# Kernel tuning notes

Hardware: AMD Instinct MI355X
Metric: run time of the kernel (lower is better)

Reference implementation:

```python
import jax, jax.numpy as jnp
import numpy as np

N_NODES = 50000
N_EDGES = 800000
NODE_DIM = 128
EDGE_DIM = 64
HIDDEN = 256


def setup_inputs() -> dict:
    key = jax.random.key(0)
    ks = jax.random.split(key, 12)
    glorot = lambda k, fi, fo: jax.random.normal(k, (fi, fo), jnp.float32) * (2.0 / (fi + fo)) ** 0.5
    return {
        "node_features": jax.random.normal(ks[0], (N_NODES, NODE_DIM), jnp.float32),
        "edge_features": jax.random.normal(ks[1], (N_EDGES, EDGE_DIM), jnp.float32),
        "src": jax.random.randint(ks[2], (N_EDGES,), 0, N_NODES),
        "dst": jax.random.randint(ks[3], (N_EDGES,), 0, N_NODES),
        # edge_update MLP: (2*node_dim + edge_dim) -> hidden -> edge_dim
        "We1": glorot(ks[4], 2 * NODE_DIM + EDGE_DIM, HIDDEN),
        "be1": jnp.zeros((HIDDEN,), jnp.float32),
        "We2": glorot(ks[5], HIDDEN, EDGE_DIM),
        "be2": jnp.zeros((EDGE_DIM,), jnp.float32),
        # node_update MLP: (node_dim + edge_dim) -> hidden -> node_dim
        "Wn1": glorot(ks[6], NODE_DIM + EDGE_DIM, HIDDEN),
        "bn1": jnp.zeros((HIDDEN,), jnp.float32),
        "Wn2": glorot(ks[7], HIDDEN, NODE_DIM),
        "bn2": jnp.zeros((NODE_DIM,), jnp.float32),
    }


def reference(node_features, edge_features, src, dst, We1, be1, We2, be2, Wn1, bn1, Wn2, bn2):
    # message: per-edge MLP on [src_h, e, dst_h]
    concat = jnp.concatenate(
        [node_features[src], edge_features, node_features[dst]], axis=1
    )  # [E, 2*node_dim + edge_dim]
    e_upd = jax.nn.relu(concat @ We1 + be1) @ We2 + be2  # [E, edge_dim]

    # reduce: sum incoming messages per destination node
    e_sum = jax.ops.segment_sum(e_upd, dst, num_segments=node_features.shape[0])  # [N, edge_dim]
    node_in = jnp.concatenate([node_features, e_sum], axis=1)  # [N, node_dim + edge_dim]
    h_new = jax.nn.relu(node_in @ Wn1 + bn1) @ Wn2 + bn2  # [N, node_dim]

    # DGL only applies reduce_func to nodes with at least one incoming edge
    deg = jax.ops.segment_sum(jnp.ones_like(dst, jnp.float32), dst, num_segments=node_features.shape[0])
    h_out = jnp.where(deg[:, None] > 0, h_new, node_features)

    # original module never writes e_updated back: returned edge features are the inputs
    return h_out, edge_features
```

## Files before the change

### kernel.cpp

```cpp
#include <hip/hip_runtime.h>

#define N_NODES 50000
#define N_EDGES 800000
#define NODE_DIM 128
#define EDGE_DIM 64
#define HIDDEN 256
#define K_N 192

typedef __attribute__((ext_vector_type(8))) short bf16x8;
typedef __attribute__((ext_vector_type(4))) float f32x4;
typedef __attribute__((ext_vector_type(16))) float f32x16;
typedef unsigned short u16;
typedef unsigned int u32;

#define MFMA16 __builtin_amdgcn_mfma_f32_16x16x32_bf16
#define MFMA32 __builtin_amdgcn_mfma_f32_32x32x16_bf16

__device__ inline u16 f2bf(float f) {
  u32 u = __builtin_bit_cast(u32, f);
  u += 0x7fffu + ((u >> 16) & 1u);
  return (u16)(u >> 16);
}
__device__ inline float bf2f(u16 u) {
  u32 x = ((u32)u) << 16;
  return __builtin_bit_cast(float, x);
}
__device__ inline u32 cvt_pk(float a, float b) {
  u32 r;
  asm("v_cvt_pk_bf16_f32 %0, %1, %2" : "=v"(r) : "v"(a), "v"(b));
  return r;
}
__device__ inline void st_bf4(u16* p, float4 v) {
  ushort4 r;
  r.x = f2bf(v.x); r.y = f2bf(v.y); r.z = f2bf(v.z); r.w = f2bf(v.w);
  *reinterpret_cast<ushort4*>(p) = r;
}

__global__ void prep_weights(const float* __restrict__ We1, const float* __restrict__ We2,
                             const float* __restrict__ Wn1, const float* __restrict__ Wn2,
                             const float* __restrict__ be2, const int* __restrict__ dst,
                             u16* __restrict__ w1st, u16* __restrict__ w1dt,
                             u16* __restrict__ w1ef, u16* __restrict__ w2y,
                             u16* __restrict__ wn1t, u16* __restrict__ wn2t,
                             float* __restrict__ b2p, int* __restrict__ hist) {
  const int stride = gridDim.x * blockDim.x;
  const int tid = blockIdx.x * blockDim.x + threadIdx.x;
  for (int i = tid; i < HIDDEN * NODE_DIM; i += stride) {
    int h = i >> 7, k = i & 127;
    w1st[i] = f2bf(We1[k * HIDDEN + h]);
    w1dt[i] = f2bf(We1[(192 + k) * HIDDEN + h]);
  }
  for (int i = tid; i < 8 * 4 * 64 * 8; i += stride) {
    int jj = i & 7;
    int l = (i >> 3) & 63;
    int kb = (i >> 9) & 3;
    int ht = i >> 11;
    int h = ht * 32 + (l & 31);
    int kloc = kb * 16 + (l >> 5) * 8 + jj;
    w1ef[i] = f2bf(We1[(128 + kloc) * HIDDEN + h]);
  }
  for (int i = tid; i < EDGE_DIM * HIDDEN; i += stride) {
    int jj = i & 7;
    int l = (i >> 3) & 63;
    int t2 = (i >> 9) & 1;
    int kb2 = i >> 10;
    int out = t2 * 32 + (l & 31);
    int hi = l >> 5;
    int k = kb2 * 16 + (jj & 3) + 8 * (jj >> 2) + 4 * hi;
    w2y[i] = f2bf(We2[k * EDGE_DIM + out]);
  }
  for (int i = tid; i < HIDDEN * K_N; i += stride) {
    int n = i / K_N, k = i % K_N;
    wn1t[i] = f2bf(Wn1[k * HIDDEN + n]);
  }
  for (int i = tid; i < NODE_DIM * HIDDEN; i += stride) {
    int n = i / HIDDEN, k = i % HIDDEN;
    wn2t[i] = f2bf(Wn2[k * NODE_DIM + n]);
  }
  for (int i = tid; i < EDGE_DIM; i += stride) {
    int t2 = i >> 5, hi = (i >> 4) & 1, r = i & 15;
    b2p[i] = be2[t2 * 32 + (r & 3) + 8 * (r >> 2) + 4 * hi];
  }
  for (int i = tid; i < N_EDGES; i += stride)
    atomicAdd(&hist[dst[i]], 1);
}

#define NB_P 782
#define SA_P 136
#define SH   264

__global__ __launch_bounds__(256) void pgemm_kernel(
    const float* __restrict__ nf, const u16* __restrict__ w1st,
    const u16* __restrict__ w1dt, const float* __restrict__ be1,
    u16* __restrict__ P_src, u16* __restrict__ P_dst)
{
  __shared__ u16 A[64 * SA_P];
  __shared__ u16 H[64 * SH];
  const int tid = threadIdx.x;
  const int n0 = blockIdx.x * 64;
  const float4* nf4 = reinterpret_cast<const float4*>(nf);

  #pragma unroll
  for (int p = 0; p < 8; ++p) {
    int i = p * 256 + tid;
    int row = i >> 5, c4 = i & 31;
    int rg = min(n0 + row, N_NODES - 1);
    float4 v = nf4[(size_t)rg * 32 + c4];
    st_bf4(&A[row * SA_P + c4 * 4], v);
  }
  __syncthreads();

  const int wave = tid >> 6, lane = tid & 63;
  const int lr = lane & 15;
  const int lk = (lane >> 4) * 8;

  for (int table = 0; table < 2; ++table) {
    const u16* w = table ? w1dt : w1st;
    u16* P = table ? P_dst : P_src;

    f32x4 acc[4][4] = {};
    #pragma unroll
    for (int kb = 0; kb < 4; ++kb) {
      const int ko = kb * 32 + lk;
      bf16x8 a[4], bb[4];
      #pragma unroll
      for (int mt = 0; mt < 4; ++mt)
        a[mt] = *reinterpret_cast<const bf16x8*>(&A[(mt * 16 + lr) * SA_P + ko]);
      #pragma unroll
      for (int nt = 0; nt < 4; ++nt)
        bb[nt] = *reinterpret_cast<const bf16x8*>(&w[(size_t)(wave * 64 + nt * 16 + lr) * 128 + ko]);
      #pragma unroll
      for (int mt = 0; mt < 4; ++mt)
        #pragma unroll
        for (int nt = 0; nt < 4; ++nt)
          acc[mt][nt] = MFMA16(a[mt], bb[nt], acc[mt][nt], 0, 0, 0);
    }
    __syncthreads();

    #pragma unroll
    for (int mt = 0; mt < 4; ++mt)
      #pragma unroll
      for (int nt = 0; nt < 4; ++nt) {
        int col = wave * 64 + nt * 16 + lr;
        float bias = table ? 0.f : be1[col];
        #pragma unroll
        for (int j = 0; j < 4; ++j) {
          int row = mt * 16 + (lane >> 4) * 4 + j;
          H[row * SH + col] = f2bf(acc[mt][nt][j] + bias);
        }
      }
    __syncthreads();

    #pragma unroll
    for (int p = 0; p < 16; ++p) {
      int u = p * 256 + tid;
      int row = u >> 6, cg = u & 63;
      int hi = cg >> 5, ht = (cg >> 2) & 7, q = cg & 3;
      int hbase = ht * 32 + 8 * q + 4 * hi;
      int n = n0 + row;
      if (n < N_NODES) {
        ushort4 v = *reinterpret_cast<const ushort4*>(&H[row * SH + hbase]);
        *reinterpret_cast<ushort4*>(&P[(size_t)n * 256 + cg * 4]) = v;
      }
    }
  }
}

#define NB_SCAN 196

__global__ void scanA_kernel(const int* __restrict__ hist, int* __restrict__ eid) {
  __shared__ int red[256];
  int gid = blockIdx.x * 256 + threadIdx.x;
  int v = (gid < N_NODES) ? hist[gid] : 0;
  red[threadIdx.x] = v;
  __syncthreads();
  for (int d = 128; d > 0; d >>= 1) {
    if (threadIdx.x < d) red[threadIdx.x] += red[threadIdx.x + d];
    __syncthreads();
  }
  if (threadIdx.x == 0) eid[blockIdx.x] = red[0];
}

__global__ void scanB_kernel(int* __restrict__ eid, int* __restrict__ off) {
  __shared__ int ssum[256];
  int tid = threadIdx.x;
  int v = (tid < NB_SCAN) ? eid[tid] : 0;
  ssum[tid] = v;
  __syncthreads();
  for (int d = 1; d < 256; d <<= 1) {
    int t = (tid >= d) ? ssum[tid - d] : 0;
    __syncthreads();
    ssum[tid] += t;
    __syncthreads();
  }
  if (tid < NB_SCAN) eid[256 + tid] = ssum[tid] - v;
  if (tid == 255) off[N_NODES] = ssum[255];
}

__global__ void scanC_kernel(const int* __restrict__ hist, const int* __restrict__ eid,
                             int* __restrict__ off, int* __restrict__ cursor,
                             float* __restrict__ e_sum) {
  __shared__ int ssum[256];
  int tid = threadIdx.x;
  int gid = blockIdx.x * 256 + tid;
  int base = eid[256 + blockIdx.x];
  int v = (gid < N_NODES) ? hist[gid] : 0;
  ssum[tid] = v;
  __syncthreads();
  for (int d = 1; d < 256; d <<= 1) {
    int t = (tid >= d) ? ssum[tid - d] : 0;
    __syncthreads();
    ssum[tid] += t;
    __syncthreads();
  }
  if (gid < N_NODES) {
    int o = base + ssum[tid] - v;
    off[gid] = o;
    cursor[gid] = o;
    float4 z = {0.f, 0.f, 0.f, 0.f};
    float4* ez = reinterpret_cast<float4*>(e_sum + (size_t)gid * 64);
    #pragma unroll
    for (int q = 0; q < 16; ++q) ez[q] = z;
  }
}

template<bool EFB>
__global__ void scatter_kernel(const int* __restrict__ src, const int* __restrict__ dst,
                               const float* __restrict__ ef,
                               int* __restrict__ cursor, int* __restrict__ eid,
                               int* __restrict__ csr_src, int* __restrict__ csr_dst,
                               u16* __restrict__ csr_efb) {
  int e = blockIdx.x * blockDim.x + threadIdx.x;
  if (e < N_EDGES) {
    int d = dst[e];
    int pos = atomicAdd(&cursor[d], 1);
    csr_src[pos] = src[e];
    csr_dst[pos] = d;
    if (EFB) {
      const float4* s = reinterpret_cast<const float4*>(ef + (size_t)e * 64);
      #pragma unroll
      for (int q = 0; q < 16; q += 2) {
        float4 v0 = s[q], v1 = s[q + 1];
        uint4 r;
        r.x = cvt_pk(v0.x, v0.y); r.y = cvt_pk(v0.z, v0.w);
        r.z = cvt_pk(v1.x, v1.y); r.w = cvt_pk(v1.z, v1.w);
        *reinterpret_cast<uint4*>(csr_efb + (size_t)pos * 64 + q * 4) = r;
      }
    } else {
      eid[pos] = e;
    }
  }
}

template<bool EFB>
__global__ __launch_bounds__(256, 4) void edge_mlp(
    const u16* __restrict__ P_src, const u16* __restrict__ P_dst,
    const float* __restrict__ ef, const u16* __restrict__ csr_efb,
    const int* __restrict__ eid, const int* __restrict__ csr_src,
    const int* __restrict__ csr_dst,
    const u16* __restrict__ w1ef, const u16* __restrict__ w2y,
    const float* __restrict__ b2p,
    float* __restrict__ e_sum, float* __restrict__ out_edge)
{
  __shared__ char shmem[33280];
  u16* W1e = reinterpret_cast<u16*>(shmem);
  float* bounce = reinterpret_cast<float*>(shmem);

  const int tid = threadIdx.x;
  const int wv = tid >> 6, lane = tid & 63;
  const int ecol = lane & 31;
  const int hi = lane >> 5;
  const int e0 = blockIdx.x * 128;
  const int pos = e0 + wv * 32 + ecol;

  {
    const uint4* s = reinterpret_cast<const uint4*>(w1ef);
    uint4* d = reinterpret_cast<uint4*>(W1e);
    #pragma unroll
    for (int j = 0; j < 8; ++j) d[j * 256 + tid] = s[j * 256 + tid];
  }

  {
    const float4* ef4 = reinterpret_cast<const float4*>(ef);
    float4* oe4 = reinterpret_cast<float4*>(out_edge);
    #pragma unroll
    for (int p = 0; p < 8; ++p) {
      size_t i = (size_t)e0 * 16 + p * 256 + tid;
      oe4[i] = ef4[i];
    }
  }

  const int srcn = csr_src[pos];
  const int dstn = csr_dst[pos];

  bf16x8 efr[4];
  if (EFB) {
    const u16* eb = csr_efb + (size_t)pos * 64 + hi * 8;
    #pragma unroll
    for (int kb = 0; kb < 4; ++kb)
      efr[kb] = *reinterpret_cast<const bf16x8*>(eb + kb * 16);
  } else {
    const int e = eid[pos];
    #pragma unroll
    for (int kb = 0; kb < 4; ++kb) {
      const float* ep = ef + (size_t)e * 64 + kb * 16 + hi * 8;
      float4 lo = *reinterpret_cast<const float4*>(ep);
      float4 hv = *reinterpret_cast<const float4*>(ep + 4);
      u32 w[4];
      w[0] = cvt_pk(lo.x, lo.y); w[1] = cvt_pk(lo.z, lo.w);
      w[2] = cvt_pk(hv.x, hv.y); w[3] = cvt_pk(hv.z, hv.w);
      efr[kb] = __builtin_bit_cast(bf16x8, *reinterpret_cast<uint4*>(w));
    }
  }

  __syncthreads();

  f32x16 acc2[2];
  #pragma unroll
  for (int t2 = 0; t2 < 2; ++t2) {
    const float* bp = b2p + t2 * 32 + hi * 16;
    #pragma unroll
    for (int r = 0; r < 16; ++r) acc2[t2][r] = bp[r];
  }

  const u16* psb = P_src + (size_t)srcn * 256 + hi * 128;
  const u16* pdb = P_dst + (size_t)dstn * 256 + hi * 128;

  bf16x8 pa0 = *reinterpret_cast<const bf16x8*>(psb);
  bf16x8 pa1 = *reinterpret_cast<const bf16x8*>(psb + 8);
  bf16x8 pd0 = *reinterpret_cast<const bf16x8*>(pdb);
  bf16x8 pd1 = *reinterpret_cast<const bf16x8*>(pdb + 8);

  #pragma unroll
  for (int ht = 0; ht < 8; ++ht) {
    bf16x8 na0, na1, nd0, nd1;
    if (ht < 7) {
      na0 = *reinterpret_cast<const bf16x8*>(psb + (ht + 1) * 16);
      na1 = *reinterpret_cast<const bf16x8*>(psb + (ht + 1) * 16 + 8);
      nd0 = *reinterpret_cast<const bf16x8*>(pdb + (ht + 1) * 16);
      nd1 = *reinterpret_cast<const bf16x8*>(pdb + (ht + 1) * 16 + 8);
    }

    f32x16 acc;
    #pragma unroll
    for (int r = 0; r < 8; ++r) {
      acc[r]     = bf2f((u16)pa0[r]) + bf2f((u16)pd0[r]);
      acc[8 + r] = bf2f((u16)pa1[r]) + bf2f((u16)pd1[r]);
    }

    #pragma unroll
    for (int kb = 0; kb < 4; ++kb) {
      bf16x8 wf = *reinterpret_cast<const bf16x8*>(W1e + ((ht * 4 + kb) * 64 + lane) * 8);
      acc = MFMA32(wf, efr[kb], acc, 0, 0, 0);
    }

    #pragma unroll
    for (int s2 = 0; s2 < 2; ++s2) {
      bf16x8 hf;
      u32* hw = reinterpret_cast<u32*>(&hf);
      #pragma unroll
      for (int m = 0; m < 4; ++m)
        hw[m] = cvt_pk(fmaxf(acc[s2 * 8 + 2 * m], 0.f),
                       fmaxf(acc[s2 * 8 + 2 * m + 1], 0.f));
      #pragma unroll
      for (int t2 = 0; t2 < 2; ++t2) {
        bf16x8 wf2 = *reinterpret_cast<const bf16x8*>(
            w2y + ((size_t)((ht * 2 + s2) * 2 + t2) * 64 + lane) * 8);
        acc2[t2] = MFMA32(wf2, hf, acc2[t2], 0, 0, 0);
      }
    }

    pa0 = na0; pa1 = na1; pd0 = nd0; pd1 = nd1;
  }

  __syncthreads();

  {
    const int lp = wv * 32 + ecol;
    #pragma unroll
    for (int t2 = 0; t2 < 2; ++t2)
      #pragma unroll
      for (int r = 0; r < 16; ++r) {
        int o = t2 * 32 + (r & 3) + 8 * (r >> 2) + 4 * hi;
        bounce[lp * 65 + o] = acc2[t2][r];
      }
  }

  {
    const int d = lane;
    const int base = wv * 32;
    float s = bounce[base * 65 + d];
    int cur = __shfl(dstn, 0, 64);
    #pragma unroll 4
    for (int i = 1; i < 32; ++i) {
      int nx = __shfl(dstn, i, 64);
      float v = bounce[(base + i) * 65 + d];
      if (nx == cur) {
        s += v;
      } else {
        atomicAdd(&e_sum[(size_t)cur * 64 + d], s);
        cur = nx;
        s = v;
      }
    }
    atomicAdd(&e_sum[(size_t)cur * 64 + d], s);
  }
}

#define SA_N 200

__global__ __launch_bounds__(256) void node_kernel(
    const float* __restrict__ nf, const float* __restrict__ e_sum,
    const int* __restrict__ hist,
    const u16* __restrict__ w1, const float* __restrict__ b1,
    const u16* __restrict__ w2, const float* __restrict__ b2,
    float* __restrict__ hout)
{
  __shared__ u16 A[64 * SH];
  const int tid = threadIdx.x;
  const int n0 = blockIdx.x * 64;

  const float4* nf4 = reinterpret_cast<const float4*>(nf);
  const float4* es4 = reinterpret_cast<const float4*>(e_sum);

  #pragma unroll
  for (int p = 0; p < 8; ++p) {
    int i = p * 256 + tid;
    int row = i >> 5, c4 = i & 31;
    int rg = min(n0 + row, N_NODES - 1);
    float4 v = nf4[(size_t)rg * 32 + c4];
    st_bf4(&A[row * SA_N + c4 * 4], v);
  }
  #pragma unroll
  for (int p = 0; p < 4; ++p) {
    int i = p * 256 + tid;
    int row = i >> 4, c4 = i & 15;
    int rg = min(n0 + row, N_NODES - 1);
    float4 v = es4[(size_t)rg * 16 + c4];
    st_bf4(&A[row * SA_N + 128 + c4 * 4], v);
  }
  __syncthreads();

  const int wave = tid >> 6, lane = tid & 63;
  const int lr = lane & 15;
  const int lk = (lane >> 4) * 8;

  f32x4 acc[4][4] = {};
  for (int kb = 0; kb < K_N / 32; ++kb) {
    const int ko = kb * 32 + lk;
    bf16x8 a[4], b[4];
    #pragma unroll
    for (int mt = 0; mt < 4; ++mt)
      a[mt] = *reinterpret_cast<const bf16x8*>(&A[(mt * 16 + lr) * SA_N + ko]);
    #pragma unroll
    for (int nt = 0; nt < 4; ++nt)
      b[nt] = *reinterpret_cast<const bf16x8*>(&w1[(size_t)(wave * 64 + nt * 16 + lr) * K_N + ko]);
    #pragma unroll
    for (int mt = 0; mt < 4; ++mt)
      #pragma unroll
      for (int nt = 0; nt < 4; ++nt)
        acc[mt][nt] = MFMA16(a[mt], b[nt], acc[mt][nt], 0, 0, 0);
  }
  __syncthreads();

  u16* H = A;
  #pragma unroll
  for (int mt = 0; mt < 4; ++mt)
    #pragma unroll
    for (int nt = 0; nt < 4; ++nt) {
      int col = wave * 64 + nt * 16 + lr;
      float bias = b1[col];
      #pragma unroll
      for (int j = 0; j < 4; ++j) {
        int row = mt * 16 + (lane >> 4) * 4 + j;
        float h = acc[mt][nt][j] + bias;
        H[row * SH + col] = f2bf(h > 0.f ? h : 0.f);
      }
    }
  __syncthreads();

  f32x4 acc2[8] = {};
  for (int kb = 0; kb < HIDDEN / 32; ++kb) {
    const int ko = kb * 32 + lk;
    bf16x8 a = *reinterpret_cast<const bf16x8*>(&H[(wave * 16 + lr) * SH + ko]);
    #pragma unroll
    for (int nt = 0; nt < 8; ++nt) {
      bf16x8 b = *reinterpret_cast<const bf16x8*>(&w2[(size_t)(nt * 16 + lr) * HIDDEN + ko]);
      acc2[nt] = MFMA16(a, b, acc2[nt], 0, 0, 0);
    }
  }
  #pragma unroll
  for (int nt = 0; nt < 8; ++nt) {
    int col = nt * 16 + lr;
    float bias = b2[col];
    #pragma unroll
    for (int j = 0; j < 4; ++j) {
      int row = wave * 16 + (lane >> 4) * 4 + j;
      int rg = n0 + row;
      if (rg < N_NODES) {
        float v = acc2[nt][j] + bias;
        hout[(size_t)rg * NODE_DIM + col] =
            (hist[rg] != 0) ? v : nf[(size_t)rg * NODE_DIM + col];
      }
    }
  }
}

extern "C" void kernel_launch(void* const* d_in, const int* in_sizes, int n_in,
                              void* d_out, int out_size, void* d_ws, size_t ws_size,
                              hipStream_t stream) {
  const float* nf  = (const float*)d_in[0];
  const float* ef  = (const float*)d_in[1];
  const int*   src = (const int*)d_in[2];
  const int*   dst = (const int*)d_in[3];
  const float* We1 = (const float*)d_in[4];
  const float* be1 = (const float*)d_in[5];
  const float* We2 = (const float*)d_in[6];
  const float* be2 = (const float*)d_in[7];
  const float* Wn1 = (const float*)d_in[8];
  const float* bn1 = (const float*)d_in[9];
  const float* Wn2 = (const float*)d_in[10];
  const float* bn2 = (const float*)d_in[11];

  float* hout = (float*)d_out;
  float* out_edge = hout + (size_t)N_NODES * NODE_DIM;

  char* ws = (char*)d_ws;
  int*   hist    = (int*)ws;
  int*   off     = (int*)(ws + 200000);
  int*   cursor  = (int*)(ws + 400016);
  int*   eid     = (int*)(ws + 600016);
  int*   csr_src = (int*)(ws + 3800016);
  int*   csr_dst = (int*)(ws + 7000016);
  float* e_sum   = (float*)(ws + 10200016);
  u16*   w1ef    = (u16*)(ws + 23000016);
  u16*   w1st    = (u16*)(ws + 23032784);
  u16*   w1dt    = (u16*)(ws + 23098320);
  u16*   w2y     = (u16*)(ws + 23163856);
  u16*   wn1t    = (u16*)(ws + 23196624);
  u16*   wn2t    = (u16*)(ws + 23294928);
  float* b2p     = (float*)(ws + 23360464);
  u16*   P_src   = (u16*)(ws + 23360720);
  u16*   P_dst   = (u16*)(ws + 48960720);
  u16*   csr_efb = (u16*)(ws + 74560720);
  const size_t NEED_EFB = 176960720;
  const int efb = (ws_size >= NEED_EFB) ? 1 : 0;

  hipMemsetAsync(hist, 0, 200000, stream);
  prep_weights<<<512, 256, 0, stream>>>(We1, We2, Wn1, Wn2, be2, dst,
                                        w1st, w1dt, w1ef, w2y, wn1t, wn2t,
                                        b2p, hist);
  pgemm_kernel<<<NB_P, 256, 0, stream>>>(nf, w1st, w1dt, be1, P_src, P_dst);
  scanA_kernel<<<NB_SCAN, 256, 0, stream>>>(hist, eid);
  scanB_kernel<<<1, 256, 0, stream>>>(eid, off);
  scanC_kernel<<<NB_SCAN, 256, 0, stream>>>(hist, eid, off, cursor, e_sum);
  if (efb) {
    scatter_kernel<true><<<(N_EDGES + 255) / 256, 256, 0, stream>>>(
        src, dst, ef, cursor, eid, csr_src, csr_dst, csr_efb);
    edge_mlp<true><<<N_EDGES / 128, 256, 0, stream>>>(
        P_src, P_dst, ef, csr_efb, eid, csr_src, csr_dst,
        w1ef, w2y, b2p, e_sum, out_edge);
  } else {
    scatter_kernel<false><<<(N_EDGES + 255) / 256, 256, 0, stream>>>(
        src, dst, ef, cursor, eid, csr_src, csr_dst, csr_efb);
    edge_mlp<false><<<N_EDGES / 128, 256, 0, stream>>>(
        P_src, P_dst, ef, csr_efb, eid, csr_src, csr_dst,
        w1ef, w2y, b2p, e_sum, out_edge);
  }
  node_kernel<<<(N_NODES + 63) / 64, 256, 0, stream>>>(nf, e_sum, hist,
                                                       wn1t, bn1, wn2t, bn2, hout);
}
```

Before: 553.7 us.

## Move edge-feature copy and bf16 conversion into a separate streaming kernel

A new grid-stride kernel copies edge features to the output and writes a bf16 copy in original edge order. The scatter kernel now writes only CSR indices plus an eid permutation, so it no longer does scattered 256-byte feature writes. The edge MLP no longer does the output copy and instead gathers bf16 features through eid, which adds an indirect, non-contiguous read per edge. The aim is to replace scattered writes and mixed copy traffic with coalesced streaming passes.

```diff
diff --git a/kernel.cpp b/kernel.cpp
--- a/kernel.cpp
+++ b/kernel.cpp
@@ -34,6 +34,27 @@
   ushort4 r;
   r.x = f2bf(v.x); r.y = f2bf(v.y); r.z = f2bf(v.z); r.w = f2bf(v.w);
   *reinterpret_cast<ushort4*>(p) = r;
+}
+
+template<bool EFB>
+__global__ __launch_bounds__(256) void convert_kernel(
+    const float* __restrict__ ef, float* __restrict__ out_edge,
+    u16* __restrict__ efb_edge) {
+  const int stride = gridDim.x * blockDim.x;
+  const float4* s = reinterpret_cast<const float4*>(ef);
+  float4* o = reinterpret_cast<float4*>(out_edge);
+  uint2* b = reinterpret_cast<uint2*>(efb_edge);
+  for (int g = blockIdx.x * blockDim.x + threadIdx.x;
+       g < N_EDGES * 16; g += stride) {
+    float4 v = s[g];
+    o[g] = v;
+    if (EFB) {
+      uint2 r;
+      r.x = cvt_pk(v.x, v.y);
+      r.y = cvt_pk(v.z, v.w);
+      b[g] = r;
+    }
+  }
 }
 
 __global__ void prep_weights(const float* __restrict__ We1, const float* __restrict__ We2,
@@ -224,43 +245,28 @@
   }
 }
 
-template<bool EFB>
 __global__ void scatter_kernel(const int* __restrict__ src, const int* __restrict__ dst,
-                               const float* __restrict__ ef,
                                int* __restrict__ cursor, int* __restrict__ eid,
-                               int* __restrict__ csr_src, int* __restrict__ csr_dst,
-                               u16* __restrict__ csr_efb) {
+                               int* __restrict__ csr_src, int* __restrict__ csr_dst) {
   int e = blockIdx.x * blockDim.x + threadIdx.x;
   if (e < N_EDGES) {
     int d = dst[e];
     int pos = atomicAdd(&cursor[d], 1);
+    eid[pos] = e;
     csr_src[pos] = src[e];
     csr_dst[pos] = d;
-    if (EFB) {
-      const float4* s = reinterpret_cast<const float4*>(ef + (size_t)e * 64);
-      #pragma unroll
-      for (int q = 0; q < 16; q += 2) {
-        float4 v0 = s[q], v1 = s[q + 1];
-        uint4 r;
-        r.x = cvt_pk(v0.x, v0.y); r.y = cvt_pk(v0.z, v0.w);
-        r.z = cvt_pk(v1.x, v1.y); r.w = cvt_pk(v1.z, v1.w);
-        *reinterpret_cast<uint4*>(csr_efb + (size_t)pos * 64 + q * 4) = r;
-      }
-    } else {
-      eid[pos] = e;
-    }
   }
 }
 
 template<bool EFB>
 __global__ __launch_bounds__(256, 4) void edge_mlp(
     const u16* __restrict__ P_src, const u16* __restrict__ P_dst,
-    const float* __restrict__ ef, const u16* __restrict__ csr_efb,
+    const float* __restrict__ ef, const u16* __restrict__ efb_edge,
     const int* __restrict__ eid, const int* __restrict__ csr_src,
     const int* __restrict__ csr_dst,
     const u16* __restrict__ w1ef, const u16* __restrict__ w2y,
     const float* __restrict__ b2p,
-    float* __restrict__ e_sum, float* __restrict__ out_edge)
+    float* __restrict__ e_sum)
 {
   __shared__ char shmem[33280];
   u16* W1e = reinterpret_cast<u16*>(shmem);
@@ -280,27 +286,17 @@
     for (int j = 0; j < 8; ++j) d[j * 256 + tid] = s[j * 256 + tid];
   }
 
-  {
-    const float4* ef4 = reinterpret_cast<const float4*>(ef);
-    float4* oe4 = reinterpret_cast<float4*>(out_edge);
-    #pragma unroll
-    for (int p = 0; p < 8; ++p) {
-      size_t i = (size_t)e0 * 16 + p * 256 + tid;
-      oe4[i] = ef4[i];
-    }
-  }
-
+  const int e    = eid[pos];
   const int srcn = csr_src[pos];
   const int dstn = csr_dst[pos];
 
   bf16x8 efr[4];
   if (EFB) {
-    const u16* eb = csr_efb + (size_t)pos * 64 + hi * 8;
+    const u16* eb = efb_edge + (size_t)e * 64 + hi * 8;
     #pragma unroll
     for (int kb = 0; kb < 4; ++kb)
       efr[kb] = *reinterpret_cast<const bf16x8*>(eb + kb * 16);
   } else {
-    const int e = eid[pos];
     #pragma unroll
     for (int kb = 0; kb < 4; ++kb) {
       const float* ep = ef + (size_t)e * 64 + kb * 16 + hi * 8;
@@ -542,7 +538,7 @@
   float* b2p     = (float*)(ws + 23360464);
   u16*   P_src   = (u16*)(ws + 23360720);
   u16*   P_dst   = (u16*)(ws + 48960720);
-  u16*   csr_efb = (u16*)(ws + 74560720);
+  u16*   efb_edge= (u16*)(ws + 74560720);
   const size_t NEED_EFB = 176960720;
   const int efb = (ws_size >= NEED_EFB) ? 1 : 0;
 
@@ -550,22 +546,22 @@
   prep_weights<<<512, 256, 0, stream>>>(We1, We2, Wn1, Wn2, be2, dst,
                                         w1st, w1dt, w1ef, w2y, wn1t, wn2t,
                                         b2p, hist);
+  if (efb) convert_kernel<true><<<2048, 256, 0, stream>>>(ef, out_edge, efb_edge);
+  else     convert_kernel<false><<<2048, 256, 0, stream>>>(ef, out_edge, efb_edge);
   pgemm_kernel<<<NB_P, 256, 0, stream>>>(nf, w1st, w1dt, be1, P_src, P_dst);
   scanA_kernel<<<NB_SCAN, 256, 0, stream>>>(hist, eid);
   scanB_kernel<<<1, 256, 0, stream>>>(eid, off);
   scanC_kernel<<<NB_SCAN, 256, 0, stream>>>(hist, eid, off, cursor, e_sum);
+  scatter_kernel<<<(N_EDGES + 255) / 256, 256, 0, stream>>>(src, dst, cursor, eid,
+                                                            csr_src, csr_dst);
   if (efb) {
-    scatter_kernel<true><<<(N_EDGES + 255) / 256, 256, 0, stream>>>(
-        src, dst, ef, cursor, eid, csr_src, csr_dst, csr_efb);
     edge_mlp<true><<<N_EDGES / 128, 256, 0, stream>>>(
-        P_src, P_dst, ef, csr_efb, eid, csr_src, csr_dst,
-        w1ef, w2y, b2p, e_sum, out_edge);
+        P_src, P_dst, ef, efb_edge, eid, csr_src, csr_dst,
+        w1ef, w2y, b2p, e_sum);
   } else {
-    scatter_kernel<false><<<(N_EDGES + 255) / 256, 256, 0, stream>>>(
-        src, dst, ef, cursor, eid, csr_src, csr_dst, csr_efb);
     edge_mlp<false><<<N_EDGES / 128, 256, 0, stream>>>(
-        P_src, P_dst, ef, csr_efb, eid, csr_src, csr_dst,
-        w1ef, w2y, b2p, e_sum, out_edge);
+        P_src, P_dst, ef, efb_edge, eid, csr_src, csr_dst,
+        w1ef, w2y, b2p, e_sum);
   }
   node_kernel<<<(N_NODES + 63) / 64, 256, 0, stream>>>(nf, e_sum, hist,
                                                        wn1t, bn1, wn2t, bn2, hout);
```

After: 512.5 us. 7.4% less time.
